# Optimization experiments

Measured on AMD Instinct MI355X. Metric: run time of the kernel, lower is better.

The kernel has to match this reference:

```python
import jax, jax.numpy as jnp
import numpy as np

N = 50000
E = 800000
G = 8
IN, HID, OUT = 128, 256, 128
BN_EPS = 1e-5


def _linear_params(key, fan_in, fan_out):
    k1, k2 = jax.random.split(key)
    s = 1.0 / np.sqrt(fan_in)
    w = jax.random.uniform(k1, (fan_out, fan_in), jnp.float32, -s, s)
    b = jax.random.uniform(k2, (fan_out,), jnp.float32, -s, s)
    return w, b


def setup_inputs() -> dict:
    key = jax.random.key(0)
    ks = jax.random.split(key, 16)
    inp = {
        "x": jax.random.normal(ks[0], (N, IN), jnp.float32),
        "src": jax.random.randint(ks[1], (E,), 0, N, jnp.int32),
        "dst": jax.random.randint(ks[2], (E,), 0, N, jnp.int32),
        "graph_ids": jnp.sort(jax.random.randint(ks[3], (N,), 0, G, jnp.int32)),
    }
    dims = [(IN, HID, HID), (HID, HID, HID), (HID, OUT, OUT)]
    for i, (d_in, d_mid, d_out) in enumerate(dims):
        kk = jax.random.split(ks[4 + i], 2)
        w1, b1 = _linear_params(kk[0], d_in, d_mid)
        w2, b2 = _linear_params(kk[1], d_mid, d_out)
        inp[f"w1_{i}"] = w1
        inp[f"b1_{i}"] = b1
        inp[f"w2_{i}"] = w2
        inp[f"b2_{i}"] = b2
        inp[f"eps_{i}"] = jnp.zeros((), jnp.float32)          # learn_eps, init 0
        inp[f"gamma_{i}"] = jnp.ones((d_out,), jnp.float32)   # BatchNorm weight
        inp[f"beta_{i}"] = jnp.zeros((d_out,), jnp.float32)   # BatchNorm bias
    return inp


def _gin_layer(h, src, dst, w1, b1, w2, b2, eps, gamma, beta):
    # GINConv: (1 + eps) * h_v + sum_{u in N(v)} h_u   (copy_u / sum)
    agg = jax.ops.segment_sum(h[src], dst, num_segments=N)
    z = (1.0 + eps) * h + agg
    # 2-layer MLP with ReLU
    z = jnp.maximum(z @ w1.T + b1, 0.0) @ w2.T + b2
    # BatchNorm1d (training-mode batch statistics, biased variance)
    mu = jnp.mean(z, axis=0)
    var = jnp.var(z, axis=0)
    return (z - mu) * jax.lax.rsqrt(var + BN_EPS) * gamma + beta


def reference(x, src, dst, graph_ids,
              w1_0, b1_0, w2_0, b2_0, eps_0, gamma_0, beta_0,
              w1_1, b1_1, w2_1, b2_1, eps_1, gamma_1, beta_1,
              w1_2, b1_2, w2_2, b2_2, eps_2, gamma_2, beta_2):
    h = _gin_layer(x, src, dst, w1_0, b1_0, w2_0, b2_0, eps_0, gamma_0, beta_0)
    h = jnp.maximum(h, 0.0)  # relu (dropout = identity in eval)
    h = _gin_layer(h, src, dst, w1_1, b1_1, w2_1, b2_1, eps_1, gamma_1, beta_1)
    h = jnp.maximum(h, 0.0)
    h = _gin_layer(h, src, dst, w1_2, b1_2, w2_2, b2_2, eps_2, gamma_2, beta_2)
    # dgl.mean_nodes: per-graph mean over nodes -> [G, OUT]
    sums = jax.ops.segment_sum(h, graph_ids, num_segments=G)
    counts = jax.ops.segment_sum(jnp.ones((N,), h.dtype), graph_ids, num_segments=G)
    return sums / jnp.maximum(counts, 1.0)[:, None]
```

## Files before the change

### kernel.cpp

```cpp
#include <hip/hip_runtime.h>

#define NG 8

typedef _Float16 half8  __attribute__((ext_vector_type(8)));
typedef float    f32x16 __attribute__((ext_vector_type(16)));


__global__ __launch_bounds__(256)
void k_cast16(const float* __restrict__ in, _Float16* __restrict__ out, int n8) {
    int i = blockIdx.x * 256 + threadIdx.x;
    if (i < n8) {
        const float4 a = *(const float4*)(in + (size_t)i * 8);
        const float4 b = *(const float4*)(in + (size_t)i * 8 + 4);
        half8 o;
        o[0] = (_Float16)a.x; o[1] = (_Float16)a.y; o[2] = (_Float16)a.z; o[3] = (_Float16)a.w;
        o[4] = (_Float16)b.x; o[5] = (_Float16)b.y; o[6] = (_Float16)b.z; o[7] = (_Float16)b.w;
        *(half8*)(out + (size_t)i * 8) = o;
    }
}

__global__ __launch_bounds__(256)
void k_castw(const float* __restrict__ w0, const float* __restrict__ w1,
             const float* __restrict__ w2, const float* __restrict__ w3,
             const float* __restrict__ w4, const float* __restrict__ w5,
             _Float16* __restrict__ o0, _Float16* __restrict__ o1,
             _Float16* __restrict__ o2, _Float16* __restrict__ o3,
             _Float16* __restrict__ o4, _Float16* __restrict__ o5) {
    int i = blockIdx.x * 256 + threadIdx.x;
    const float* in; _Float16* out; int off, lgC, K;
    if      (i <  4096) { in = w0; out = o0; off = 0;     lgC = 8; K = 128; }
    else if (i < 12288) { in = w1; out = o1; off = 4096;  lgC = 8; K = 256; }
    else if (i < 20480) { in = w2; out = o2; off = 12288; lgC = 8; K = 256; }
    else if (i < 28672) { in = w3; out = o3; off = 20480; lgC = 8; K = 256; }
    else if (i < 32768) { in = w4; out = o4; off = 28672; lgC = 7; K = 256; }
    else if (i < 34816) { in = w5; out = o5; off = 32768; lgC = 7; K = 128; }
    else return;
    int j = i - off;
    int kslot = j >> lgC;
    int c = j & ((1 << lgC) - 1);
    const float* s = in + (size_t)c * K + kslot * 8;
    const float4 a = *(const float4*)(s);
    const float4 b = *(const float4*)(s + 4);
    half8 o;
    o[0] = (_Float16)a.x; o[1] = (_Float16)a.y; o[2] = (_Float16)a.z; o[3] = (_Float16)a.w;
    o[4] = (_Float16)b.x; o[5] = (_Float16)b.y; o[6] = (_Float16)b.z; o[7] = (_Float16)b.w;
    *(half8*)(out + (size_t)j * 8) = o;
}


__global__ __launch_bounds__(256)
void k_deg(const int* __restrict__ dst, int* __restrict__ deg, int E) {
    int i = blockIdx.x * 256 + threadIdx.x;
    if (i < E) atomicAdd(&deg[dst[i]], 1);
}

__global__ __launch_bounds__(1024)
void k_scan_a(const int* __restrict__ deg, int* __restrict__ incl,
              int* __restrict__ bsum, int n) {
    __shared__ int s[1024];
    int t = threadIdx.x;
    int base = blockIdx.x * 1024;
    int v = (base + t < n) ? deg[base + t] : 0;
    s[t] = v;
    __syncthreads();
    for (int off = 1; off < 1024; off <<= 1) {
        int x = 0;
        if (t >= off) x = s[t - off];
        __syncthreads();
        if (t >= off) s[t] += x;
        __syncthreads();
    }
    if (base + t < n) incl[base + t] = s[t];
    if (t == 1023) bsum[blockIdx.x] = s[1023];
}

__global__ void k_scan_b(int* bsum, int nb) {
    if (threadIdx.x == 0 && blockIdx.x == 0) {
        int run = 0;
        for (int i = 0; i < nb; ++i) { int v = bsum[i]; bsum[i] = run; run += v; }
    }
}

__global__ __launch_bounds__(256)
void k_scan_c(const int* __restrict__ incl, const int* __restrict__ deg,
              const int* __restrict__ bsum, int* __restrict__ rowp, int n) {
    int i = blockIdx.x * 256 + threadIdx.x;
    if (i < n) rowp[i] = incl[i] - deg[i] + bsum[i >> 10];
}

__global__ __launch_bounds__(256)
void k_scatter(const int* __restrict__ src, const int* __restrict__ dst,
               const int* __restrict__ rowp, int* __restrict__ cur,
               int* __restrict__ ss, int E) {
    int i = blockIdx.x * 256 + threadIdx.x;
    if (i < E) {
        int d = dst[i];
        int pos = rowp[d] + atomicAdd(&cur[d], 1);
        ss[pos] = src[i];
    }
}


template<int K, bool AFFINE>
__global__ __launch_bounds__(256)
void k_agg16(const _Float16* __restrict__ h, const int* __restrict__ rowp,
             const int* __restrict__ deg, const int* __restrict__ ss,
             const float* __restrict__ eps, const float* __restrict__ scp,
             const float* __restrict__ shp, _Float16* __restrict__ z, int n) {
    constexpr int TPN = K / 8;
    constexpr int NPB = 256 / TPN;
    int node = blockIdx.x * NPB + threadIdx.x / TPN;
    int lane = threadIdx.x % TPN;
    if (node >= n) return;
    float e1 = 1.0f + eps[0];
    const int c0 = lane * 8;
    float sc[8], sh[8];
    if (AFFINE) {
#pragma unroll
        for (int e = 0; e < 8; ++e) { sc[e] = scp[c0 + e]; sh[e] = shp[c0 + e]; }
    }
    size_t base = (size_t)node * K + c0;
    half8 v = *(const half8*)(h + base);
    float a[8];
#pragma unroll
    for (int e = 0; e < 8; ++e) {
        float f = (float)v[e];
        if (AFFINE) f = fmaxf(f * sc[e] + sh[e], 0.0f);
        a[e] = f * e1;
    }
    int s  = rowp[node];
    int dn = deg[node];
    int j = 0;
    for (; j + 4 <= dn; j += 4) {
        int u0 = ss[s + j], u1 = ss[s + j + 1], u2 = ss[s + j + 2], u3 = ss[s + j + 3];
        half8 h0 = *(const half8*)(h + (size_t)u0 * K + c0);
        half8 h1 = *(const half8*)(h + (size_t)u1 * K + c0);
        half8 h2 = *(const half8*)(h + (size_t)u2 * K + c0);
        half8 h3 = *(const half8*)(h + (size_t)u3 * K + c0);
#pragma unroll
        for (int e = 0; e < 8; ++e) {
            float f0 = (float)h0[e], f1 = (float)h1[e];
            float f2 = (float)h2[e], f3 = (float)h3[e];
            if (AFFINE) {
                f0 = fmaxf(f0 * sc[e] + sh[e], 0.0f);
                f1 = fmaxf(f1 * sc[e] + sh[e], 0.0f);
                f2 = fmaxf(f2 * sc[e] + sh[e], 0.0f);
                f3 = fmaxf(f3 * sc[e] + sh[e], 0.0f);
            }
            a[e] += (f0 + f1) + (f2 + f3);
        }
    }
    for (; j < dn; ++j) {
        int u = ss[s + j];
        half8 hv = *(const half8*)(h + (size_t)u * K + c0);
#pragma unroll
        for (int e = 0; e < 8; ++e) {
            float f = (float)hv[e];
            if (AFFINE) f = fmaxf(f * sc[e] + sh[e], 0.0f);
            a[e] += f;
        }
    }
    half8 o;
#pragma unroll
    for (int e = 0; e < 8; ++e) o[e] = (_Float16)a[e];
    *(half8*)(z + base) = o;
}


template<int K, int MID, int MOUT>
__global__ __launch_bounds__(512)
void k_mlp3(const _Float16* __restrict__ A, const _Float16* __restrict__ W1,
            const float* __restrict__ b1, const _Float16* __restrict__ W2,
            const float* __restrict__ b2, _Float16* __restrict__ C,
            float* __restrict__ partial, int n, int ntiles) {
    constexpr int NK1 = K / 16;
    constexpr int NK2 = MID / 16;
    constexpr int MF1 = (MID == 256) ? 2 : 1;
    constexpr int MF2 = (MOUT == 256) ? 2 : 1;
    constexpr int NLD = K / 64;
    __shared__ char As[64 * 512];
    __shared__ char Ys[64 * 512];
    __shared__ char tbs[8 * 2304];
    const int tid  = threadIdx.x;
    const int lane = tid & 63;
    const int wid  = tid >> 6;
    const int lo   = lane & 31;
    const int hi   = lane >> 5;

    const int wc1 = (MID == 256) ? wid : (wid & 3);
    const int wr1 = (MID == 256) ? 0   : (wid >> 2);
    const int colbase1 = wc1 * 32;
    const int wc2 = (MOUT == 256) ? wid : (wid & 3);
    const int wr2 = (MOUT == 256) ? 0   : (wid >> 2);
    const int colbase2 = wc2 * 32;

    half8 w1f[NK1], w2f[NK2];
#pragma unroll
    for (int ks = 0; ks < NK1; ++ks)
        w1f[ks] = *(const half8*)(W1 + ((size_t)(ks * 2 + hi) * MID + colbase1 + lo) * 8);
#pragma unroll
    for (int ks = 0; ks < NK2; ++ks)
        w2f[ks] = *(const half8*)(W2 + ((size_t)(ks * 2 + hi) * MOUT + colbase2 + lo) * 8);
    const float bb1 = b1[colbase1 + lo];
    const float bb2 = b2[colbase2 + lo];

    const int sr = tid >> 3;
    const int sl = tid & 7;
    const int g  = lane & 3;
    const int rl = lane >> 2;
    char* tb = tbs + wid * 2304;

    float s[8], q[8];
#pragma unroll
    for (int e = 0; e < 8; ++e) { s[e] = 0.f; q[e] = 0.f; }

    int tile = blockIdx.x;
    uint4 ar[NLD];
    if (tile < ntiles) {
        int ga = tile * 64 + sr; if (ga > n - 1) ga = n - 1;
        const char* Ab = (const char*)(A + (size_t)ga * K);
#pragma unroll
        for (int i = 0; i < NLD; ++i) ar[i] = *(const uint4*)(Ab + (sl + i * 8) * 16);
    }

    for (; tile < ntiles; tile += gridDim.x) {
        const int brow = tile * 64;

#pragma unroll
        for (int i = 0; i < NLD; ++i)
            *(uint4*)(As + sr * 512 + (((sl + i * 8) ^ (sr & 31)) << 4)) = ar[i];
        int nt = tile + gridDim.x;
        if (nt < ntiles) {
            int ga = nt * 64 + sr; if (ga > n - 1) ga = n - 1;
            const char* Ab = (const char*)(A + (size_t)ga * K);
#pragma unroll
            for (int i = 0; i < NLD; ++i) ar[i] = *(const uint4*)(Ab + (sl + i * 8) * 16);
        }
        __syncthreads();

        f32x16 acc1[MF1];
#pragma unroll
        for (int mf = 0; mf < MF1; ++mf)
#pragma unroll
            for (int e = 0; e < 16; ++e) acc1[mf][e] = 0.0f;
#pragma unroll
        for (int ks = 0; ks < NK1; ++ks) {
#pragma unroll
            for (int mf = 0; mf < MF1; ++mf) {
                int r = ((wr1 + mf) << 5) + lo;
                half8 af = *(const half8*)(As + r * 512 + ((ks * 32 + hi * 16) ^ ((r & 31) << 4)));
                acc1[mf] = __builtin_amdgcn_mfma_f32_32x32x16_f16(af, w1f[ks], acc1[mf], 0, 0, 0);
            }
        }
#pragma unroll
        for (int mf = 0; mf < MF1; ++mf) {
            int rb = ((wr1 + mf) << 5) + (hi << 2);
#pragma unroll
            for (int j = 0; j < 16; ++j) {
                int r = rb + (j & 3) + ((j >> 2) << 3);
                float v = fmaxf(acc1[mf][j] + bb1, 0.0f);
                *(_Float16*)(Ys + r * 512 + (((colbase1 + lo) * 2) ^ ((r & 31) << 4))) = (_Float16)v;
            }
        }
        __syncthreads();

        f32x16 acc2[MF2];
#pragma unroll
        for (int mf = 0; mf < MF2; ++mf)
#pragma unroll
            for (int e = 0; e < 16; ++e) acc2[mf][e] = 0.0f;
#pragma unroll
        for (int ks = 0; ks < NK2; ++ks) {
#pragma unroll
            for (int mf = 0; mf < MF2; ++mf) {
                int r = ((wr2 + mf) << 5) + lo;
                half8 af = *(const half8*)(Ys + r * 512 + ((ks * 32 + hi * 16) ^ ((r & 31) << 4)));
                acc2[mf] = __builtin_amdgcn_mfma_f32_32x32x16_f16(af, w2f[ks], acc2[mf], 0, 0, 0);
            }
        }

#pragma unroll
        for (int mf = 0; mf < MF2; ++mf) {
#pragma unroll
            for (int j = 0; j < 16; ++j) {
                int tr = (j & 3) + ((j >> 2) << 3) + (hi << 2);
                *(_Float16*)(tb + tr * 72 + lo * 2) = (_Float16)(acc2[mf][j] + bb2);
            }
#pragma unroll
            for (int it = 0; it < 2; ++it) {
                int lr = it * 16 + rl;
                int grow = brow + ((wr2 + mf) << 5) + lr;
                half8 v = *(const half8*)(tb + lr * 72 + g * 16);
                if (grow < n) {
                    *(half8*)(C + (size_t)grow * MOUT + colbase2 + g * 8) = v;
#pragma unroll
                    for (int e = 0; e < 8; ++e) { float f = (float)v[e]; s[e] += f; q[e] += f * f; }
                }
            }
        }
    }

#pragma unroll
    for (int e = 0; e < 8; ++e) {
        for (int mk = 4; mk < 64; mk <<= 1) {
            s[e] += __shfl_xor(s[e], mk, 64);
            q[e] += __shfl_xor(q[e], mk, 64);
        }
    }
    if (lane < 4) {
        float* p = partial + ((size_t)blockIdx.x * 2 + wr2) * (2 * MOUT);
#pragma unroll
        for (int e = 0; e < 8; ++e) {
            p[colbase2 + lane * 8 + e]        = s[e];
            p[MOUT + colbase2 + lane * 8 + e] = q[e];
        }
    }
}


template<int M>
__global__ __launch_bounds__(256)
void k_bnred(const float* __restrict__ partial, const float* __restrict__ gamma,
             const float* __restrict__ beta, float* __restrict__ scale,
             float* __restrict__ shift, int n, int count, int step) {
    const int w = threadIdx.x >> 6, lane = threadIdx.x & 63;
    const int c = blockIdx.x * 4 + w;
    float s = 0.f, q = 0.f;
    for (int b = lane; b < count; b += 64) {
        const float* p = partial + (size_t)(b * step) * (2 * M);
        s += p[c];
        q += p[M + c];
    }
#pragma unroll
    for (int mk = 1; mk < 64; mk <<= 1) {
        s += __shfl_xor(s, mk, 64);
        q += __shfl_xor(q, mk, 64);
    }
    if (lane == 0) {
        float invN = 1.0f / (float)n;
        float mean = s * invN;
        float var  = q * invN - mean * mean;
        float sc   = rsqrtf(var + 1e-5f) * gamma[c];
        scale[c] = sc;
        shift[c] = beta[c] - mean * sc;
    }
}


__global__ __launch_bounds__(256)
void k_readout_bn(const _Float16* __restrict__ z, const float* __restrict__ scale,
                  const float* __restrict__ shift, const int* __restrict__ gid,
                  float* __restrict__ gsum, int* __restrict__ gcnt, int n) {
    __shared__ float ls[NG * 128];
    __shared__ int   lc[NG];
    for (int i = threadIdx.x; i < NG * 128; i += 256) ls[i] = 0.0f;
    if (threadIdx.x < NG) lc[threadIdx.x] = 0;
    __syncthreads();
    int c  = threadIdx.x & 127;
    int ro = threadIdx.x >> 7;
    const float sc = scale[c];
    const float sh = shift[c];
    float acc = 0.0f;
    int cnt = 0, curg = -1;
    for (int r = blockIdx.x * 2 + ro; r < n; r += gridDim.x * 2) {
        int g = gid[r];
        if (g != curg) {
            if (curg >= 0) {
                atomicAdd(&ls[curg * 128 + c], acc);
                if (c == 0) atomicAdd(&lc[curg], cnt);
            }
            curg = g; acc = 0.0f; cnt = 0;
        }
        acc += (float)z[(size_t)r * 128 + c] * sc + sh;
        ++cnt;
    }
    if (curg >= 0) {
        atomicAdd(&ls[curg * 128 + c], acc);
        if (c == 0) atomicAdd(&lc[curg], cnt);
    }
    __syncthreads();
    for (int i = threadIdx.x; i < NG * 128; i += 256) atomicAdd(&gsum[i], ls[i]);
    if (threadIdx.x < NG) atomicAdd(&gcnt[threadIdx.x], lc[threadIdx.x]);
}

__global__ void k_final(const float* __restrict__ gsum, const int* __restrict__ gcnt,
                        float* __restrict__ out) {
    int i = blockIdx.x * 256 + threadIdx.x;
    if (i < NG * 128) {
        int g = i >> 7;
        out[i] = gsum[i] / fmaxf((float)gcnt[g], 1.0f);
    }
}


extern "C" void kernel_launch(void* const* d_in, const int* in_sizes, int n_in,
                              void* d_out, int out_size, void* d_ws, size_t ws_size,
                              hipStream_t stream) {
    const float* x   = (const float*)d_in[0];
    const int*   src = (const int*)d_in[1];
    const int*   dst = (const int*)d_in[2];
    const int*   gid = (const int*)d_in[3];
    const int n = in_sizes[0] / 128;
    const int E = in_sizes[1];

    auto align = [](size_t o) { return (o + 255) & ~(size_t)255; };
    char* ws = (char*)d_ws;
    size_t off = 0;
    const size_t SZ_H = align((size_t)n * 256 * sizeof(_Float16));
    const size_t SZ_I = align((size_t)n * sizeof(int));
    const int gx = (n + 63) / 64;
    const int NBLK = 256;

    _Float16* h0 = (_Float16*)(ws + off); off += align((size_t)n * 128 * sizeof(_Float16));
    _Float16* P0 = (_Float16*)(ws + off); off += SZ_H;
    _Float16* P1 = (_Float16*)(ws + off); off += SZ_H;
    int*   deg  = (int*)(ws + off);   off += SZ_I;
    int*   incl = (int*)(ws + off);   off += SZ_I;
    int*   rowp = (int*)(ws + off);   off += SZ_I;
    int*   cur  = (int*)(ws + off);   off += SZ_I;
    int*   bsum = (int*)(ws + off);   off += 256 * sizeof(int);
    int*   ss   = (int*)(ws + off);   off += align((size_t)E * sizeof(int));
    float* partial = (float*)(ws + off); off += align((size_t)(2 * NBLK) * 2 * 256 * sizeof(float));
    float* scale   = (float*)(ws + off); off += align(256 * sizeof(float));
    float* shiftb  = (float*)(ws + off); off += align(256 * sizeof(float));
    float* gsum = (float*)(ws + off); off += align(NG * 128 * sizeof(float));
    int*   gcnt = (int*)(ws + off);   off += align(NG * sizeof(int));
    _Float16* wh[6];
    for (int i = 0; i < 6; ++i) { wh[i] = (_Float16*)(ws + off); off += align(65536 * sizeof(_Float16)); }

    k_cast16<<<(n * 128 / 8 + 255) / 256, 256, 0, stream>>>(x, h0, n * 128 / 8);
    k_castw<<<136, 256, 0, stream>>>(
        (const float*)d_in[4], (const float*)d_in[6],
        (const float*)d_in[11], (const float*)d_in[13],
        (const float*)d_in[18], (const float*)d_in[20],
        wh[0], wh[1], wh[2], wh[3], wh[4], wh[5]);

    hipMemsetAsync(deg, 0, (size_t)n * sizeof(int), stream);
    k_deg<<<(E + 255) / 256, 256, 0, stream>>>(dst, deg, E);
    int nb = (n + 1023) / 1024;
    k_scan_a<<<nb, 1024, 0, stream>>>(deg, incl, bsum, n);
    k_scan_b<<<1, 1, 0, stream>>>(bsum, nb);
    k_scan_c<<<(n + 255) / 256, 256, 0, stream>>>(incl, deg, bsum, rowp, n);
    hipMemsetAsync(cur, 0, (size_t)n * sizeof(int), stream);
    k_scatter<<<(E + 255) / 256, 256, 0, stream>>>(src, dst, rowp, cur, ss, E);

    for (int L = 0; L < 3; ++L) {
        const int base = 4 + 7 * L;
        const float* b1    = (const float*)d_in[base + 1];
        const float* b2    = (const float*)d_in[base + 3];
        const float* eps   = (const float*)d_in[base + 4];
        const float* gamma = (const float*)d_in[base + 5];
        const float* beta  = (const float*)d_in[base + 6];

        if (L == 0) {
            k_agg16<128, false><<<(n + 15) / 16, 256, 0, stream>>>(
                h0, rowp, deg, ss, eps, nullptr, nullptr, P1, n);
            k_mlp3<128, 256, 256><<<NBLK, 512, 0, stream>>>(P1, wh[0], b1, wh[1], b2, P0, partial, n, gx);
            k_bnred<256><<<64, 256, 0, stream>>>(partial, gamma, beta, scale, shiftb, n, NBLK, 2);
        } else if (L == 1) {
            k_agg16<256, true><<<(n + 7) / 8, 256, 0, stream>>>(
                P0, rowp, deg, ss, eps, scale, shiftb, P1, n);
            k_mlp3<256, 256, 256><<<NBLK, 512, 0, stream>>>(P1, wh[2], b1, wh[3], b2, P0, partial, n, gx);
            k_bnred<256><<<64, 256, 0, stream>>>(partial, gamma, beta, scale, shiftb, n, NBLK, 2);
        } else {
            k_agg16<256, true><<<(n + 7) / 8, 256, 0, stream>>>(
                P0, rowp, deg, ss, eps, scale, shiftb, P1, n);
            k_mlp3<256, 128, 128><<<NBLK, 512, 0, stream>>>(P1, wh[4], b1, wh[5], b2, P0, partial, n, gx);
            k_bnred<128><<<32, 256, 0, stream>>>(partial, gamma, beta, scale, shiftb, n, 2 * NBLK, 1);
        }
    }

    hipMemsetAsync(gsum, 0, NG * 128 * sizeof(float), stream);
    hipMemsetAsync(gcnt, 0, NG * sizeof(int), stream);
    k_readout_bn<<<256, 256, 0, stream>>>(P0, scale, shiftb, gid, gsum, gcnt, n);
    k_final<<<4, 256, 0, stream>>>(gsum, gcnt, (float*)d_out);
}
```

Baseline: 416.4 us.

## Alias MLP transpose buffer onto Ys, double MLP grid, rewrite readout deterministically

The MLP kernel's per-wave transpose scratch now reuses the Ys shared buffer, with an extra barrier, which cuts LDS per block and may allow more resident blocks. The MLP grid grows from 256 to 512 persistent blocks. The readout becomes vectorised half8 loads with per-block partials written to global memory and reduced by a final kernel, removing the memsets and global atomics. The trade-offs are an extra barrier per tile, per-element shared atomics in the readout, and a serial reduction over 1024 partials in the final kernel.

Measured after the change: 732.8 us. 76.0% more time.

```diff
diff --git a/kernel.cpp b/kernel.cpp
--- a/kernel.cpp
+++ b/kernel.cpp
@@ -180,7 +180,6 @@
     constexpr int NLD = K / 64;
     __shared__ char As[64 * 512];
     __shared__ char Ys[64 * 512];
-    __shared__ char tbs[8 * 2304];
     const int tid  = threadIdx.x;
     const int lane = tid & 63;
     const int wid  = tid >> 6;
@@ -208,7 +207,7 @@
     const int sl = tid & 7;
     const int g  = lane & 3;
     const int rl = lane >> 2;
-    char* tb = tbs + wid * 2304;
+    char* tb = Ys + wid * 2304;
 
     float s[8], q[8];
 #pragma unroll
@@ -278,6 +277,7 @@
                 acc2[mf] = __builtin_amdgcn_mfma_f32_32x32x16_f16(af, w2f[ks], acc2[mf], 0, 0, 0);
             }
         }
+        __syncthreads();
 
 #pragma unroll
         for (int mf = 0; mf < MF2; ++mf) {
@@ -348,48 +348,45 @@
 
 
 __global__ __launch_bounds__(256)
-void k_readout_bn(const _Float16* __restrict__ z, const float* __restrict__ scale,
-                  const float* __restrict__ shift, const int* __restrict__ gid,
-                  float* __restrict__ gsum, int* __restrict__ gcnt, int n) {
+void k_readout2(const _Float16* __restrict__ z, const float* __restrict__ scale,
+                const float* __restrict__ shift, const int* __restrict__ gid,
+                float* __restrict__ rpart, int* __restrict__ rcnt, int n) {
     __shared__ float ls[NG * 128];
     __shared__ int   lc[NG];
     for (int i = threadIdx.x; i < NG * 128; i += 256) ls[i] = 0.0f;
     if (threadIdx.x < NG) lc[threadIdx.x] = 0;
     __syncthreads();
-    int c  = threadIdx.x & 127;
-    int ro = threadIdx.x >> 7;
-    const float sc = scale[c];
-    const float sh = shift[c];
-    float acc = 0.0f;
-    int cnt = 0, curg = -1;
-    for (int r = blockIdx.x * 2 + ro; r < n; r += gridDim.x * 2) {
+    const int c16 = threadIdx.x & 15;
+    const int ro  = threadIdx.x >> 4;
+    const int c0  = c16 * 8;
+    float sc[8], sh[8];
+#pragma unroll
+    for (int e = 0; e < 8; ++e) { sc[e] = scale[c0 + e]; sh[e] = shift[c0 + e]; }
+    for (int r = blockIdx.x * 16 + ro; r < n; r += gridDim.x * 16) {
         int g = gid[r];
-        if (g != curg) {
-            if (curg >= 0) {
-                atomicAdd(&ls[curg * 128 + c], acc);
-                if (c == 0) atomicAdd(&lc[curg], cnt);
-            }
-            curg = g; acc = 0.0f; cnt = 0;
-        }
-        acc += (float)z[(size_t)r * 128 + c] * sc + sh;
-        ++cnt;
-    }
-    if (curg >= 0) {
-        atomicAdd(&ls[curg * 128 + c], acc);
-        if (c == 0) atomicAdd(&lc[curg], cnt);
+        half8 v = *(const half8*)(z + (size_t)r * 128 + c0);
+#pragma unroll
+        for (int e = 0; e < 8; ++e)
+            atomicAdd(&ls[g * 128 + c0 + e], (float)v[e] * sc[e] + sh[e]);
+        if (c16 == 0) atomicAdd(&lc[g], 1);
     }
     __syncthreads();
-    for (int i = threadIdx.x; i < NG * 128; i += 256) atomicAdd(&gsum[i], ls[i]);
-    if (threadIdx.x < NG) atomicAdd(&gcnt[threadIdx.x], lc[threadIdx.x]);
-}
-
-__global__ void k_final(const float* __restrict__ gsum, const int* __restrict__ gcnt,
-                        float* __restrict__ out) {
-    int i = blockIdx.x * 256 + threadIdx.x;
-    if (i < NG * 128) {
-        int g = i >> 7;
-        out[i] = gsum[i] / fmaxf((float)gcnt[g], 1.0f);
-    }
+    float* p = rpart + (size_t)blockIdx.x * (NG * 128);
+    for (int i = threadIdx.x; i < NG * 128; i += 256) p[i] = ls[i];
+    if (threadIdx.x < NG) rcnt[blockIdx.x * NG + threadIdx.x] = lc[threadIdx.x];
+}
+
+__global__ __launch_bounds__(256)
+void k_final2(const float* __restrict__ rpart, const int* __restrict__ rcnt,
+              float* __restrict__ out, int nbr) {
+    int i = blockIdx.x * 256 + threadIdx.x;
+    if (i >= NG * 128) return;
+    int g = i >> 7;
+    float s = 0.0f;
+    for (int b = 0; b < nbr; ++b) s += rpart[(size_t)b * (NG * 128) + i];
+    int cnt = 0;
+    for (int b = 0; b < nbr; ++b) cnt += rcnt[b * NG + g];
+    out[i] = s / fmaxf((float)cnt, 1.0f);
 }
 
 
@@ -409,7 +406,8 @@
     const size_t SZ_H = align((size_t)n * 256 * sizeof(_Float16));
     const size_t SZ_I = align((size_t)n * sizeof(int));
     const int gx = (n + 63) / 64;
-    const int NBLK = 256;
+    const int NBLK = 512;
+    const int RB   = 1024;
 
     _Float16* h0 = (_Float16*)(ws + off); off += align((size_t)n * 128 * sizeof(_Float16));
     _Float16* P0 = (_Float16*)(ws + off); off += SZ_H;
@@ -423,8 +421,8 @@
     float* partial = (float*)(ws + off); off += align((size_t)(2 * NBLK) * 2 * 256 * sizeof(float));
     float* scale   = (float*)(ws + off); off += align(256 * sizeof(float));
     float* shiftb  = (float*)(ws + off); off += align(256 * sizeof(float));
-    float* gsum = (float*)(ws + off); off += align(NG * 128 * sizeof(float));
-    int*   gcnt = (int*)(ws + off);   off += align(NG * sizeof(int));
+    float* rpart = (float*)(ws + off); off += align((size_t)RB * NG * 128 * sizeof(float));
+    int*   rcnt  = (int*)(ws + off);  off += align((size_t)RB * NG * sizeof(int));
     _Float16* wh[6];
     for (int i = 0; i < 6; ++i) { wh[i] = (_Float16*)(ws + off); off += align(65536 * sizeof(_Float16)); }
 
@@ -470,8 +468,6 @@
         }
     }
 
-    hipMemsetAsync(gsum, 0, NG * 128 * sizeof(float), stream);
-    hipMemsetAsync(gcnt, 0, NG * sizeof(int), stream);
-    k_readout_bn<<<256, 256, 0, stream>>>(P0, scale, shiftb, gid, gsum, gcnt, n);
-    k_final<<<4, 256, 0, stream>>>(gsum, gcnt, (float*)d_out);
-}
+    k_readout2<<<RB, 256, 0, stream>>>(P0, scale, shiftb, gid, rpart, rcnt, n);
+    k_final2<<<4, 256, 0, stream>>>(rpart, rcnt, (float*)d_out, RB);
+}
```
